# Performance work log

Hardware: AMD Instinct MI355X
Metric: run time of the kernel (lower is better)

The kernel has to match this reference:

```python
import jax, jax.numpy as jnp
import numpy as np

B, S, E, H = 4, 1024, 1024, 16
HD = E // H  # 64 = 2**6


def _hadamard(n_qubits):
    h = np.array([[1.0, 1.0], [1.0, -1.0]]) / np.sqrt(2.0)
    m = h
    for _ in range(n_qubits - 1):
        m = np.kron(m, h)
    return m.astype(np.float32)


def _entanglement_mask(num_heads, seed=42):
    rng = np.random.RandomState(seed)
    mask = np.eye(num_heads, dtype=np.float32)
    perm = rng.permutation(num_heads)
    for i in range(0, num_heads - 1, 2):
        h1, h2 = perm[i], perm[i + 1]
        mask[h1, h2] = 0.2
        mask[h2, h1] = 0.2
    return mask


def setup_inputs() -> dict:
    key = jax.random.key(0)
    ks = jax.random.split(key, 12)
    sc = 0.02
    return {
        "query": jax.random.normal(ks[0], (B, S, E), jnp.float32),
        "key": jax.random.normal(ks[1], (B, S, E), jnp.float32),
        "value": jax.random.normal(ks[2], (B, S, E), jnp.float32),
        "Wq": jax.random.normal(ks[3], (E, E), jnp.float32) * sc,
        "bq": jnp.zeros((E,), jnp.float32),
        "Wk": jax.random.normal(ks[4], (E, E), jnp.float32) * sc,
        "bk": jnp.zeros((E,), jnp.float32),
        "Wv": jax.random.normal(ks[5], (E, E), jnp.float32) * sc,
        "bv": jnp.zeros((E,), jnp.float32),
        "Wo": jax.random.normal(ks[6], (E, E), jnp.float32) * sc,
        "bo": jnp.zeros((E,), jnp.float32),
        "phase": jax.random.normal(ks[7], (H, HD), jnp.float32) * 0.02,
        "hadamard": jnp.asarray(_hadamard(6)),            # [HD, HD]
        "ent_mask": jnp.asarray(_entanglement_mask(H)),  # [H, H]
    }


def reference(query, key, value, Wq, bq, Wk, bk, Wv, bv, Wo, bo, phase, hadamard, ent_mask):
    b, sq, _ = query.shape
    sk = key.shape[1]
    # projections (torch Linear: x @ W.T + b), split heads -> [b, h, s, d]
    q = (query @ Wq.T + bq).reshape(b, sq, H, HD).transpose(0, 2, 1, 3)
    k = (key @ Wk.T + bk).reshape(b, sk, H, HD).transpose(0, 2, 1, 3)
    v = (value @ Wv.T + bv).reshape(b, sk, H, HD).transpose(0, 2, 1, 3)
    # superposition: right-multiply by Hadamard on head_dim
    q = jnp.einsum('bhsd,de->bhse', q, hadamard)
    k = jnp.einsum('bhsd,de->bhse', k, hadamard)
    # phase encoding: real(x * exp(+/- i*phi)) == x * cos(phi)
    cphi = jnp.cos(phase)[None, :, None, :]  # [1, h, 1, d]
    q = q * cphi
    k = k * cphi
    # attention
    attn = jnp.einsum('bhqd,bhkd->bhqk', q, k) / jnp.sqrt(jnp.float32(HD))
    probs = jax.nn.softmax(attn, axis=-1)
    # entanglement: mix heads post-softmax
    probs = jnp.einsum('bhqk,hg->bgqk', probs, ent_mask)
    # context and output projection
    ctx = jnp.einsum('bhqk,bhkd->bhqd', probs, v)
    ctx = ctx.transpose(0, 2, 1, 3).reshape(b, sq, E)
    out = ctx @ Wo.T + bo
    return out, probs
```

## Files before the change

### kernel.cpp

```cpp
#include <hip/hip_runtime.h>
#include <hip/hip_bf16.h>


#define S_ 1024
#define E_ 1024
#define H_ 16
#define HD_ 64
#define B_ 4

typedef __bf16 bf16x8 __attribute__((ext_vector_type(8)));
typedef __bf16 bf16x4 __attribute__((ext_vector_type(4)));
typedef float f32x4 __attribute__((ext_vector_type(4)));

__device__ inline bf16x8 ld8(const __bf16* p) { return *(const bf16x8*)p; }
__device__ inline bf16x8 ld8(const float* p) {
    f32x4 u0 = *(const f32x4*)p;
    f32x4 u1 = *(const f32x4*)(p + 4);
    bf16x8 r;
    r[0] = (__bf16)u0[0]; r[1] = (__bf16)u0[1]; r[2] = (__bf16)u0[2]; r[3] = (__bf16)u0[3];
    r[4] = (__bf16)u1[0]; r[5] = (__bf16)u1[1]; r[6] = (__bf16)u1[2]; r[7] = (__bf16)u1[3];
    return r;
}
__device__ inline void stc(__bf16* p, float v) { *p = (__bf16)v; }
__device__ inline void stc(float* p, float v) { *p = v; }

__device__ inline void gld16(const __bf16* g, __bf16* l) {
    __builtin_amdgcn_global_load_lds(
        (const __attribute__((address_space(1))) unsigned int*)g,
        (__attribute__((address_space(3))) unsigned int*)l,
        16, 0, 0);
}

__global__ __launch_bounds__(256) void cast3_kernel(
    const float* __restrict__ a, const float* __restrict__ b2, const float* __restrict__ c,
    __bf16* __restrict__ oa, __bf16* __restrict__ ob, __bf16* __restrict__ oc)
{
    int which = blockIdx.y;
    const float* in = which == 0 ? a : (which == 1 ? b2 : c);
    __bf16* out = which == 0 ? oa : (which == 1 ? ob : oc);
    long i = ((long)blockIdx.x * 256 + threadIdx.x) * 8;
    f32x4 u0 = *(const f32x4*)(in + i);
    f32x4 u1 = *(const f32x4*)(in + i + 4);
    bf16x8 r;
    r[0] = (__bf16)u0[0]; r[1] = (__bf16)u0[1]; r[2] = (__bf16)u0[2]; r[3] = (__bf16)u0[3];
    r[4] = (__bf16)u1[0]; r[5] = (__bf16)u1[1]; r[6] = (__bf16)u1[2]; r[7] = (__bf16)u1[3];
    *(bf16x8*)(out + i) = r;
}

__global__ __launch_bounds__(256) void eff_weight_kernel(
    const float* __restrict__ W, const float* __restrict__ had,
    const float* __restrict__ phase, __bf16* __restrict__ Weff)
{
    int g = blockIdx.x * 256 + threadIdx.x;
    int row = g >> 10;
    int j = g & 1023;
    int h = row >> 6, e = row & 63;
    float c = cosf(phase[row]);
    float acc = 0.f;
#pragma unroll 8
    for (int d = 0; d < 64; ++d)
        acc += had[d * 64 + e] * W[(((h << 6) + d) << 10) + j];
    Weff[g] = (__bf16)(acc * c);
}

__global__ __launch_bounds__(256) void eff_bias_kernel(
    const float* __restrict__ bvec, const float* __restrict__ had,
    const float* __restrict__ phase, float* __restrict__ beff)
{
    int row = blockIdx.x * 256 + threadIdx.x;
    int e = row & 63, h = row >> 6;
    float acc = 0.f;
#pragma unroll 8
    for (int d = 0; d < 64; ++d)
        acc += had[d * 64 + e] * bvec[(h << 6) + d];
    beff[row] = acc * cosf(phase[row]);
}

template <typename AT, typename CT>
__global__ __launch_bounds__(256) void gemm_bt(
    const AT* __restrict__ A, long lda, long sA1, long sA2,
    const __bf16* __restrict__ B, long ldb, long sB1, long sB2,
    CT* __restrict__ C, long ldc, long sC1, long sC2,
    const float* __restrict__ bias, int K, float alpha)
{
    int z = blockIdx.z, z1 = z >> 4, z2 = z & 15;
    const AT* Ab = A + (long)z1 * sA1 + (long)z2 * sA2;
    const __bf16* Bb = B + (long)z1 * sB1 + (long)z2 * sB2;
    CT* Cb = C + (long)z1 * sC1 + (long)z2 * sC2;

    int w = threadIdx.x >> 6, l = threadIdx.x & 63;
    int q = l >> 4, lm = l & 15;
    int ko = q * 8;
    long r0 = (long)blockIdx.x * 64 + (w >> 1) * 32 + lm;
    long c0 = (long)blockIdx.y * 64 + (w & 1) * 32 + lm;

    f32x4 acc00 = {0.f, 0.f, 0.f, 0.f};
    f32x4 acc01 = acc00, acc10 = acc00, acc11 = acc00;
    const AT* pa0 = Ab + r0 * lda + ko;
    const AT* pa1 = pa0 + 16 * lda;
    const __bf16* pb0 = Bb + c0 * ldb + ko;
    const __bf16* pb1 = pb0 + 16 * ldb;

    for (int k = 0; k < K; k += 32) {
        bf16x8 a0 = ld8(pa0 + k);
        bf16x8 a1 = ld8(pa1 + k);
        bf16x8 b0 = ld8(pb0 + k);
        bf16x8 b1 = ld8(pb1 + k);
        acc00 = __builtin_amdgcn_mfma_f32_16x16x32_bf16(a0, b0, acc00, 0, 0, 0);
        acc01 = __builtin_amdgcn_mfma_f32_16x16x32_bf16(a0, b1, acc01, 0, 0, 0);
        acc10 = __builtin_amdgcn_mfma_f32_16x16x32_bf16(a1, b0, acc10, 0, 0, 0);
        acc11 = __builtin_amdgcn_mfma_f32_16x16x32_bf16(a1, b1, acc11, 0, 0, 0);
    }

    f32x4 accs[2][2] = {{acc00, acc01}, {acc10, acc11}};
    long rbase = (long)blockIdx.x * 64 + (w >> 1) * 32 + q * 4;
    long cbase = (long)blockIdx.y * 64 + (w & 1) * 32 + lm;
#pragma unroll
    for (int i = 0; i < 2; ++i)
#pragma unroll
        for (int j = 0; j < 2; ++j) {
            long col = cbase + j * 16;
            float bv = bias ? bias[col] : 0.f;
#pragma unroll
            for (int rr = 0; rr < 4; ++rr) {
                long row = rbase + i * 16 + rr;
                stc(&Cb[row * ldc + col], accs[i][j][rr] * alpha + bv);
            }
        }
}

template <typename CT>
__global__ __launch_bounds__(256) void gemm_bt_tiled(
    const __bf16* __restrict__ A, const __bf16* __restrict__ B,
    CT* __restrict__ C, const float* __restrict__ bias, int K, int ldc)
{
    __shared__ __bf16 As[128 * 32];
    __shared__ __bf16 Bs[128 * 32];
    int t = threadIdx.x;
    int w = t >> 6, l = t & 63;
    int lm = l & 15, kq = l >> 4;
    int wm = w >> 1, wn = w & 1;
    long row0 = (long)blockIdx.x * 128;
    long col0 = (long)blockIdx.y * 128;

    int srow = l >> 2, skol = (l & 3) * 8;
    int c0i = w * 2, c1i = w * 2 + 1;
    const __bf16* gA0 = A + (row0 + c0i * 16 + srow) * (long)K + skol;
    const __bf16* gA1 = A + (row0 + c1i * 16 + srow) * (long)K + skol;
    const __bf16* gB0 = B + (col0 + c0i * 16 + srow) * (long)K + skol;
    const __bf16* gB1 = B + (col0 + c1i * 16 + srow) * (long)K + skol;
    __bf16* lA0 = &As[c0i * 512];
    __bf16* lA1 = &As[c1i * 512];
    __bf16* lB0 = &Bs[c0i * 512];
    __bf16* lB1 = &Bs[c1i * 512];

    f32x4 acc[4][4] = {};
    for (int k0 = 0; k0 < K; k0 += 32) {
        gld16(gA0 + k0, lA0);
        gld16(gA1 + k0, lA1);
        gld16(gB0 + k0, lB0);
        gld16(gB1 + k0, lB1);
        __syncthreads();
        bf16x8 af[4], bfr[4];
#pragma unroll
        for (int i = 0; i < 4; ++i)
            af[i] = *(const bf16x8*)&As[(wm * 64 + i * 16 + lm) * 32 + kq * 8];
#pragma unroll
        for (int j = 0; j < 4; ++j)
            bfr[j] = *(const bf16x8*)&Bs[(wn * 64 + j * 16 + lm) * 32 + kq * 8];
#pragma unroll
        for (int i = 0; i < 4; ++i)
#pragma unroll
            for (int j = 0; j < 4; ++j)
                acc[i][j] = __builtin_amdgcn_mfma_f32_16x16x32_bf16(af[i], bfr[j], acc[i][j], 0, 0, 0);
        __syncthreads();
    }

    long rbase = row0 + wm * 64 + kq * 4;
    long cbase = col0 + wn * 64 + lm;
#pragma unroll
    for (int i = 0; i < 4; ++i)
#pragma unroll
        for (int j = 0; j < 4; ++j) {
            long col = cbase + j * 16;
            float bv = bias ? bias[col] : 0.f;
#pragma unroll
            for (int rr = 0; rr < 4; ++rr) {
                long row = rbase + i * 16 + rr;
                stc(&C[row * (long)ldc + col], acc[i][j][rr] + bv);
            }
        }
}

__global__ __launch_bounds__(256) void transpose_v(
    const __bf16* __restrict__ v2, __bf16* __restrict__ vt)
{
    int blk = blockIdx.x;
    int st = blk & 15;
    int h = (blk >> 4) & 15;
    int b = blk >> 8;
    __shared__ __bf16 tile[64][72];
    int t = threadIdx.x;
    int sl = t >> 2, dc = (t & 3) * 16;
    const __bf16* src = v2 + ((long)(b * 1024 + st * 64 + sl)) * 1024 + h * 64 + dc;
    bf16x8 u0 = *(const bf16x8*)src;
    bf16x8 u1 = *(const bf16x8*)(src + 8);
#pragma unroll
    for (int j = 0; j < 8; ++j) { tile[sl][dc + j] = u0[j]; tile[sl][dc + 8 + j] = u1[j]; }
    __syncthreads();
    int dl = t >> 2, scn = (t & 3) * 16;
    __bf16* dst = vt + ((long)((b * 16 + h) * 64 + dl)) * 1024 + st * 64 + scn;
    bf16x8 o0, o1;
#pragma unroll
    for (int j = 0; j < 8; ++j) { o0[j] = tile[scn + j][dl]; o1[j] = tile[scn + 8 + j][dl]; }
    *(bf16x8*)dst = o0;
    *(bf16x8*)(dst + 8) = o1;
}

__global__ __launch_bounds__(256) void attn_kernel(
    const __bf16* __restrict__ Q2, const __bf16* __restrict__ K2,
    float* __restrict__ probs)
{
    __shared__ float redm[16][4] __attribute__((aligned(16)));
    __shared__ float reds[16][4] __attribute__((aligned(16)));
    int z = blockIdx.z;
    int b = z >> 4, h = z & 15;
    int qt = blockIdx.x;
    int w = threadIdx.x >> 6, l = threadIdx.x & 63;
    int q = l >> 4, lm = l & 15;
    int ko = q * 8;

    const __bf16* Qb = Q2 + (long)b * S_ * E_ + (long)h * 64;
    const __bf16* Kb = K2 + (long)b * S_ * E_ + (long)h * 64;

    const __bf16* pa = Qb + (long)(qt * 16 + lm) * E_ + ko;
    bf16x8 a0 = *(const bf16x8*)pa;
    bf16x8 a1 = *(const bf16x8*)(pa + 32);

    f32x4 acc[16];
#pragma unroll
    for (int f = 0; f < 16; ++f) {
        int n0 = w * 256 + f * 16;
        const __bf16* pb = Kb + (long)(n0 + lm) * E_ + ko;
        bf16x8 b0 = *(const bf16x8*)pb;
        bf16x8 b1 = *(const bf16x8*)(pb + 32);
        f32x4 tt = {0.f, 0.f, 0.f, 0.f};
        tt = __builtin_amdgcn_mfma_f32_16x16x32_bf16(a0, b0, tt, 0, 0, 0);
        tt = __builtin_amdgcn_mfma_f32_16x16x32_bf16(a1, b1, tt, 0, 0, 0);
        acc[f] = tt;
    }

    float m[4];
#pragma unroll
    for (int rr = 0; rr < 4; ++rr) {
        float mm = acc[0][rr];
#pragma unroll
        for (int f = 1; f < 16; ++f) mm = fmaxf(mm, acc[f][rr]);
#pragma unroll
        for (int off = 1; off < 16; off <<= 1) mm = fmaxf(mm, __shfl_xor(mm, off, 64));
        m[rr] = mm;
    }
    if (lm == 0) {
#pragma unroll
        for (int rr = 0; rr < 4; ++rr) redm[q * 4 + rr][w] = m[rr];
    }
    __syncthreads();
#pragma unroll
    for (int rr = 0; rr < 4; ++rr) {
        f32x4 v = *(const f32x4*)redm[q * 4 + rr];
        m[rr] = fmaxf(fmaxf(v[0], v[1]), fmaxf(v[2], v[3]));
    }

    float s[4] = {0.f, 0.f, 0.f, 0.f};
#pragma unroll
    for (int f = 0; f < 16; ++f) {
        f32x4 tt = acc[f];
#pragma unroll
        for (int rr = 0; rr < 4; ++rr) {
            float p = __expf((tt[rr] - m[rr]) * 0.125f);
            tt[rr] = p;
            s[rr] += p;
        }
        acc[f] = tt;
    }
#pragma unroll
    for (int rr = 0; rr < 4; ++rr) {
#pragma unroll
        for (int off = 1; off < 16; off <<= 1) s[rr] += __shfl_xor(s[rr], off, 64);
    }
    if (lm == 0) {
#pragma unroll
        for (int rr = 0; rr < 4; ++rr) reds[q * 4 + rr][w] = s[rr];
    }
    __syncthreads();
    float inv[4];
#pragma unroll
    for (int rr = 0; rr < 4; ++rr) {
        f32x4 v = *(const f32x4*)reds[q * 4 + rr];
        inv[rr] = 1.0f / (v[0] + v[1] + v[2] + v[3]);
    }

    float* prow = probs + (long)z * S_ * S_ + (long)(qt * 16) * S_;
#pragma unroll
    for (int f = 0; f < 16; ++f) {
        int col = w * 256 + f * 16 + lm;
#pragma unroll
        for (int rr = 0; rr < 4; ++rr)
            prow[(long)(q * 4 + rr) * S_ + col] = acc[f][rr] * inv[rr];
    }
}

__global__ __launch_bounds__(256) void mix_kernel(
    float* __restrict__ probs, const float* __restrict__ mask)
{
    __shared__ float mm[256];
    int t = threadIdx.x;
    mm[t] = mask[t];
    __syncthreads();
    long gid = (long)blockIdx.x * 256 + t;
    long e4 = gid * 4;
    int b = (int)(e4 >> 20);
    long rem = e4 & 1048575;
    float* base = probs + ((long)b << 24) + rem;
    f32x4 acc[16];
#pragma unroll
    for (int g = 0; g < 16; ++g) acc[g] = (f32x4){0.f, 0.f, 0.f, 0.f};
#pragma unroll
    for (int hh = 0; hh < 16; ++hh) {
        f32x4 vv = *(const f32x4*)(base + ((long)hh << 20));
#pragma unroll
        for (int g = 0; g < 16; ++g) acc[g] += vv * mm[hh * 16 + g];
    }
#pragma unroll
    for (int g = 0; g < 16; ++g) *(f32x4*)(base + ((long)g << 20)) = acc[g];
}

extern "C" void kernel_launch(void* const* d_in, const int* in_sizes, int n_in,
                              void* d_out, int out_size, void* d_ws, size_t ws_size,
                              hipStream_t stream) {
    (void)in_sizes; (void)n_in; (void)out_size; (void)ws_size;
    const float* query = (const float*)d_in[0];
    const float* key   = (const float*)d_in[1];
    const float* value = (const float*)d_in[2];
    const float* Wq    = (const float*)d_in[3];
    const float* bq    = (const float*)d_in[4];
    const float* Wk    = (const float*)d_in[5];
    const float* bk    = (const float*)d_in[6];
    const float* Wv    = (const float*)d_in[7];
    const float* bv    = (const float*)d_in[8];
    const float* Wo    = (const float*)d_in[9];
    const float* bo    = (const float*)d_in[10];
    const float* phase = (const float*)d_in[11];
    const float* had   = (const float*)d_in[12];
    const float* mask  = (const float*)d_in[13];

    __bf16* wqe  = (__bf16*)d_ws;
    __bf16* wke  = wqe + 1048576;
    __bf16* wv16 = wke + 1048576;
    __bf16* wo16 = wv16 + 1048576;
    float*  bqe  = (float*)(wo16 + 1048576);
    float*  bke  = bqe + 1024;
    __bf16* q16  = (__bf16*)(bke + 1024);
    __bf16* k16  = q16 + 4194304;
    __bf16* v16  = k16 + 4194304;
    __bf16* q2   = v16 + 4194304;
    __bf16* k2   = q2 + 4194304;
    __bf16* v2   = k2 + 4194304;
    __bf16* vt   = k16;
    __bf16* ctx  = q16;

    float* out   = (float*)d_out;
    float* probs = out + 4194304;

    cast3_kernel<<<dim3(2048, 3), 256, 0, stream>>>(query, key, value, q16, k16, v16);
    cast3_kernel<<<dim3(512, 2), 256, 0, stream>>>(Wv, Wo, nullptr, wv16, wo16, nullptr);

    eff_weight_kernel<<<4096, 256, 0, stream>>>(Wq, had, phase, wqe);
    eff_weight_kernel<<<4096, 256, 0, stream>>>(Wk, had, phase, wke);
    eff_bias_kernel<<<4, 256, 0, stream>>>(bq, had, phase, bqe);
    eff_bias_kernel<<<4, 256, 0, stream>>>(bk, had, phase, bke);

    dim3 gt(32, 8, 1);
    gemm_bt_tiled<__bf16><<<gt, 256, 0, stream>>>(q16, wqe, q2, bqe, 1024, 1024);
    gemm_bt_tiled<__bf16><<<gt, 256, 0, stream>>>(k16, wke, k2, bke, 1024, 1024);
    gemm_bt_tiled<__bf16><<<gt, 256, 0, stream>>>(v16, wv16, v2, bv, 1024, 1024);

    transpose_v<<<1024, 256, 0, stream>>>(v2, vt);

    attn_kernel<<<dim3(64, 1, 64), 256, 0, stream>>>(q2, k2, probs);

    mix_kernel<<<4096, 256, 0, stream>>>(probs, mask);

    gemm_bt<float, __bf16><<<dim3(16, 1, 64), 256, 0, stream>>>(
        probs, 1024, 16777216, 1048576,
        vt,    1024, 1048576,  65536,
        ctx,   1024, 1048576,  64,
        nullptr, 1024, 1.0f);

    gemm_bt_tiled<float><<<gt, 256, 0, stream>>>(ctx, wo16, out, bo, 1024, 1024);
}
```

Measured before the change: 755.0 us.

## Fuse head-mixing with P@V and batch QKV projections into single launches

Replaces the separate head-mix pass and the batched P@V GEMM with one kernel. It mixes the probabilities across heads in registers, writes the mixed probs out once, stages a bf16 copy in swizzled LDS, and runs the MFMA product against transposed V directly. This is meant to remove a full fp32 re-read of the 256 MB probs tensor. The Q/K/V projection GEMMs and the effective-weight and bias prep are each merged into one launch via grid dimensions. The trade-off is a small grid (256 blocks of 512 threads) with narrow 8-byte loads, which may limit memory-level parallelism.

```diff
diff --git a/kernel.cpp b/kernel.cpp
--- a/kernel.cpp
+++ b/kernel.cpp
@@ -10,17 +10,10 @@
 
 typedef __bf16 bf16x8 __attribute__((ext_vector_type(8)));
 typedef __bf16 bf16x4 __attribute__((ext_vector_type(4)));
+typedef __bf16 bf16x2 __attribute__((ext_vector_type(2)));
 typedef float f32x4 __attribute__((ext_vector_type(4)));
-
-__device__ inline bf16x8 ld8(const __bf16* p) { return *(const bf16x8*)p; }
-__device__ inline bf16x8 ld8(const float* p) {
-    f32x4 u0 = *(const f32x4*)p;
-    f32x4 u1 = *(const f32x4*)(p + 4);
-    bf16x8 r;
-    r[0] = (__bf16)u0[0]; r[1] = (__bf16)u0[1]; r[2] = (__bf16)u0[2]; r[3] = (__bf16)u0[3];
-    r[4] = (__bf16)u1[0]; r[5] = (__bf16)u1[1]; r[6] = (__bf16)u1[2]; r[7] = (__bf16)u1[3];
-    return r;
-}
+typedef float f32x2 __attribute__((ext_vector_type(2)));
+
 __device__ inline void stc(__bf16* p, float v) { *p = (__bf16)v; }
 __device__ inline void stc(float* p, float v) { *p = v; }
 
@@ -47,10 +40,13 @@
     *(bf16x8*)(out + i) = r;
 }
 
-__global__ __launch_bounds__(256) void eff_weight_kernel(
-    const float* __restrict__ W, const float* __restrict__ had,
-    const float* __restrict__ phase, __bf16* __restrict__ Weff)
-{
+__global__ __launch_bounds__(256) void eff_weight2_kernel(
+    const float* __restrict__ Wq, const float* __restrict__ Wk,
+    const float* __restrict__ had, const float* __restrict__ phase,
+    __bf16* __restrict__ wqe, __bf16* __restrict__ wke)
+{
+    const float* W = blockIdx.y ? Wk : Wq;
+    __bf16* Weff = blockIdx.y ? wke : wqe;
     int g = blockIdx.x * 256 + threadIdx.x;
     int row = g >> 10;
     int j = g & 1023;
@@ -63,10 +59,13 @@
     Weff[g] = (__bf16)(acc * c);
 }
 
-__global__ __launch_bounds__(256) void eff_bias_kernel(
-    const float* __restrict__ bvec, const float* __restrict__ had,
-    const float* __restrict__ phase, float* __restrict__ beff)
-{
+__global__ __launch_bounds__(256) void eff_bias2_kernel(
+    const float* __restrict__ bq, const float* __restrict__ bk,
+    const float* __restrict__ had, const float* __restrict__ phase,
+    float* __restrict__ bqe, float* __restrict__ bke)
+{
+    const float* bvec = blockIdx.y ? bk : bq;
+    float* beff = blockIdx.y ? bke : bqe;
     int row = blockIdx.x * 256 + threadIdx.x;
     int e = row & 63, h = row >> 6;
     float acc = 0.f;
@@ -76,61 +75,8 @@
     beff[row] = acc * cosf(phase[row]);
 }
 
-template <typename AT, typename CT>
-__global__ __launch_bounds__(256) void gemm_bt(
-    const AT* __restrict__ A, long lda, long sA1, long sA2,
-    const __bf16* __restrict__ B, long ldb, long sB1, long sB2,
-    CT* __restrict__ C, long ldc, long sC1, long sC2,
-    const float* __restrict__ bias, int K, float alpha)
-{
-    int z = blockIdx.z, z1 = z >> 4, z2 = z & 15;
-    const AT* Ab = A + (long)z1 * sA1 + (long)z2 * sA2;
-    const __bf16* Bb = B + (long)z1 * sB1 + (long)z2 * sB2;
-    CT* Cb = C + (long)z1 * sC1 + (long)z2 * sC2;
-
-    int w = threadIdx.x >> 6, l = threadIdx.x & 63;
-    int q = l >> 4, lm = l & 15;
-    int ko = q * 8;
-    long r0 = (long)blockIdx.x * 64 + (w >> 1) * 32 + lm;
-    long c0 = (long)blockIdx.y * 64 + (w & 1) * 32 + lm;
-
-    f32x4 acc00 = {0.f, 0.f, 0.f, 0.f};
-    f32x4 acc01 = acc00, acc10 = acc00, acc11 = acc00;
-    const AT* pa0 = Ab + r0 * lda + ko;
-    const AT* pa1 = pa0 + 16 * lda;
-    const __bf16* pb0 = Bb + c0 * ldb + ko;
-    const __bf16* pb1 = pb0 + 16 * ldb;
-
-    for (int k = 0; k < K; k += 32) {
-        bf16x8 a0 = ld8(pa0 + k);
-        bf16x8 a1 = ld8(pa1 + k);
-        bf16x8 b0 = ld8(pb0 + k);
-        bf16x8 b1 = ld8(pb1 + k);
-        acc00 = __builtin_amdgcn_mfma_f32_16x16x32_bf16(a0, b0, acc00, 0, 0, 0);
-        acc01 = __builtin_amdgcn_mfma_f32_16x16x32_bf16(a0, b1, acc01, 0, 0, 0);
-        acc10 = __builtin_amdgcn_mfma_f32_16x16x32_bf16(a1, b0, acc10, 0, 0, 0);
-        acc11 = __builtin_amdgcn_mfma_f32_16x16x32_bf16(a1, b1, acc11, 0, 0, 0);
-    }
-
-    f32x4 accs[2][2] = {{acc00, acc01}, {acc10, acc11}};
-    long rbase = (long)blockIdx.x * 64 + (w >> 1) * 32 + q * 4;
-    long cbase = (long)blockIdx.y * 64 + (w & 1) * 32 + lm;
-#pragma unroll
-    for (int i = 0; i < 2; ++i)
-#pragma unroll
-        for (int j = 0; j < 2; ++j) {
-            long col = cbase + j * 16;
-            float bv = bias ? bias[col] : 0.f;
-#pragma unroll
-            for (int rr = 0; rr < 4; ++rr) {
-                long row = rbase + i * 16 + rr;
-                stc(&Cb[row * ldc + col], accs[i][j][rr] * alpha + bv);
-            }
-        }
-}
-
 template <typename CT>
-__global__ __launch_bounds__(256) void gemm_bt_tiled(
+__device__ __forceinline__ void gemm_bt_body(
     const __bf16* __restrict__ A, const __bf16* __restrict__ B,
     CT* __restrict__ C, const float* __restrict__ bias, int K, int ldc)
 {
@@ -192,6 +138,27 @@
         }
 }
 
+template <typename CT>
+__global__ __launch_bounds__(256) void gemm_one(
+    const __bf16* __restrict__ A, const __bf16* __restrict__ B,
+    CT* __restrict__ C, const float* __restrict__ bias, int K, int ldc)
+{
+    gemm_bt_body<CT>(A, B, C, bias, K, ldc);
+}
+
+__global__ __launch_bounds__(256) void gemm_qkv(
+    const __bf16* __restrict__ A0, const __bf16* __restrict__ B0, __bf16* __restrict__ C0, const float* __restrict__ bi0,
+    const __bf16* __restrict__ A1, const __bf16* __restrict__ B1, __bf16* __restrict__ C1, const float* __restrict__ bi1,
+    const __bf16* __restrict__ A2, const __bf16* __restrict__ B2, __bf16* __restrict__ C2, const float* __restrict__ bi2)
+{
+    int z = blockIdx.z;
+    const __bf16* A = z == 0 ? A0 : (z == 1 ? A1 : A2);
+    const __bf16* B = z == 0 ? B0 : (z == 1 ? B1 : B2);
+    __bf16* C = z == 0 ? C0 : (z == 1 ? C1 : C2);
+    const float* bi = z == 0 ? bi0 : (z == 1 ? bi1 : bi2);
+    gemm_bt_body<__bf16>(A, B, C, bi, 1024, 1024);
+}
+
 __global__ __launch_bounds__(256) void transpose_v(
     const __bf16* __restrict__ v2, __bf16* __restrict__ vt)
 {
@@ -310,29 +277,73 @@
     }
 }
 
-__global__ __launch_bounds__(256) void mix_kernel(
-    float* __restrict__ probs, const float* __restrict__ mask)
-{
-    __shared__ float mm[256];
+__global__ __launch_bounds__(512) void mixpv_kernel(
+    float* __restrict__ probs, const __bf16* __restrict__ vt,
+    const float* __restrict__ mask, __bf16* __restrict__ ctx)
+{
+    __shared__ __bf16 pm[16 * 16 * 64];
     int t = threadIdx.x;
-    mm[t] = mask[t];
-    __syncthreads();
-    long gid = (long)blockIdx.x * 256 + t;
-    long e4 = gid * 4;
-    int b = (int)(e4 >> 20);
-    long rem = e4 & 1048575;
-    float* base = probs + ((long)b << 24) + rem;
-    f32x4 acc[16];
-#pragma unroll
-    for (int g = 0; g < 16; ++g) acc[g] = (f32x4){0.f, 0.f, 0.f, 0.f};
-#pragma unroll
-    for (int hh = 0; hh < 16; ++hh) {
-        f32x4 vv = *(const f32x4*)(base + ((long)hh << 20));
-#pragma unroll
-        for (int g = 0; g < 16; ++g) acc[g] += vv * mm[hh * 16 + g];
-    }
-#pragma unroll
-    for (int g = 0; g < 16; ++g) *(f32x4*)(base + ((long)g << 20)) = acc[g];
+    int w = t >> 6, l = t & 63;
+    int lm = l & 15, kq = l >> 4;
+    int b = blockIdx.z, qt = blockIdx.x;
+
+    int mq = t >> 5, mkk = (t & 31) * 2;
+    float* pbase = probs + ((long)b << 24) + (long)(qt * 16 + mq) * 1024 + mkk;
+    const __bf16* vtb = vt + ((long)(b * 16 + w * 2)) * 65536;
+    int swzw = (mq & 7) << 4;
+    int swzr = (lm & 7) << 4;
+
+    f32x4 acc[2][4] = {};
+
+    for (int c = 0; c < 16; ++c) {
+        int k0 = c * 64;
+        f32x2 mout[16];
+#pragma unroll
+        for (int g = 0; g < 16; ++g) mout[g] = (f32x2){0.f, 0.f};
+#pragma unroll
+        for (int hh = 0; hh < 16; ++hh) {
+            f32x2 vv = *(const f32x2*)(pbase + ((long)hh << 20) + k0);
+#pragma unroll
+            for (int g = 0; g < 16; ++g) {
+                float cw = mask[hh * 16 + g];
+                if (cw != 0.f) mout[g] += vv * cw;
+            }
+        }
+        __syncthreads();
+#pragma unroll
+        for (int g = 0; g < 16; ++g) {
+            *(f32x2*)(pbase + ((long)g << 20) + k0) = mout[g];
+            bf16x2 pv; pv[0] = (__bf16)mout[g][0]; pv[1] = (__bf16)mout[g][1];
+            int cb = (mkk * 2) ^ swzw;
+            *(bf16x2*)&pm[(g * 16 + mq) * 64 + (cb >> 1)] = pv;
+        }
+        __syncthreads();
+#pragma unroll
+        for (int gl = 0; gl < 2; ++gl) {
+            int rowb = ((w * 2 + gl) * 16 + lm) * 64;
+            bf16x8 a0 = *(const bf16x8*)&pm[rowb + (((kq * 16) ^ swzr) >> 1)];
+            bf16x8 a1 = *(const bf16x8*)&pm[rowb + (((64 + kq * 16) ^ swzr) >> 1)];
+            const __bf16* vg = vtb + gl * 65536 + k0 + kq * 8;
+#pragma unroll
+            for (int j = 0; j < 4; ++j) {
+                bf16x8 b0 = *(const bf16x8*)(vg + (j * 16 + lm) * 1024);
+                bf16x8 b1 = *(const bf16x8*)(vg + (j * 16 + lm) * 1024 + 32);
+                acc[gl][j] = __builtin_amdgcn_mfma_f32_16x16x32_bf16(a0, b0, acc[gl][j], 0, 0, 0);
+                acc[gl][j] = __builtin_amdgcn_mfma_f32_16x16x32_bf16(a1, b1, acc[gl][j], 0, 0, 0);
+            }
+        }
+    }
+
+    long rb = (long)(b * 1024 + qt * 16 + kq * 4);
+#pragma unroll
+    for (int gl = 0; gl < 2; ++gl)
+#pragma unroll
+        for (int j = 0; j < 4; ++j) {
+            long colb = (long)((w * 2 + gl) * 64 + j * 16 + lm);
+#pragma unroll
+            for (int rr = 0; rr < 4; ++rr)
+                ctx[(rb + rr) * 1024 + colb] = (__bf16)acc[gl][j][rr];
+        }
 }
 
 extern "C" void kernel_launch(void* const* d_in, const int* in_sizes, int n_in,
@@ -375,27 +386,19 @@
     cast3_kernel<<<dim3(2048, 3), 256, 0, stream>>>(query, key, value, q16, k16, v16);
     cast3_kernel<<<dim3(512, 2), 256, 0, stream>>>(Wv, Wo, nullptr, wv16, wo16, nullptr);
 
-    eff_weight_kernel<<<4096, 256, 0, stream>>>(Wq, had, phase, wqe);
-    eff_weight_kernel<<<4096, 256, 0, stream>>>(Wk, had, phase, wke);
-    eff_bias_kernel<<<4, 256, 0, stream>>>(bq, had, phase, bqe);
-    eff_bias_kernel<<<4, 256, 0, stream>>>(bk, had, phase, bke);
-
-    dim3 gt(32, 8, 1);
-    gemm_bt_tiled<__bf16><<<gt, 256, 0, stream>>>(q16, wqe, q2, bqe, 1024, 1024);
-    gemm_bt_tiled<__bf16><<<gt, 256, 0, stream>>>(k16, wke, k2, bke, 1024, 1024);
-    gemm_bt_tiled<__bf16><<<gt, 256, 0, stream>>>(v16, wv16, v2, bv, 1024, 1024);
+    eff_weight2_kernel<<<dim3(4096, 2), 256, 0, stream>>>(Wq, Wk, had, phase, wqe, wke);
+    eff_bias2_kernel<<<dim3(4, 2), 256, 0, stream>>>(bq, bk, had, phase, bqe, bke);
+
+    gemm_qkv<<<dim3(32, 8, 3), 256, 0, stream>>>(
+        q16, wqe, q2, bqe,
+        k16, wke, k2, bke,
+        v16, wv16, v2, bv);
 
     transpose_v<<<1024, 256, 0, stream>>>(v2, vt);
 
     attn_kernel<<<dim3(64, 1, 64), 256, 0, stream>>>(q2, k2, probs);
 
-    mix_kernel<<<4096, 256, 0, stream>>>(probs, mask);
-
-    gemm_bt<float, __bf16><<<dim3(16, 1, 64), 256, 0, stream>>>(
-        probs, 1024, 16777216, 1048576,
-        vt,    1024, 1048576,  65536,
-        ctx,   1024, 1048576,  64,
-        nullptr, 1024, 1.0f);
-
-    gemm_bt_tiled<float><<<gt, 256, 0, stream>>>(ctx, wo16, out, bo, 1024, 1024);
-}
+    mixpv_kernel<<<dim3(64, 1, 4), 512, 0, stream>>>(probs, vt, mask, ctx);
+
+    gemm_one<float><<<dim3(32, 8), 256, 0, stream>>>(ctx, wo16, out, bo, 1024, 1024);
+}
```

Result: slower. 873.6 us (+15.7%).
